# Optimization experiments

Measured on AMD Instinct MI355X. Metric: run time of the kernel, lower is better.

The kernel has to match this reference:

```python
import jax, jax.numpy as jnp
import numpy as np

N = 100000
E = 1600000
IN_CH = 128
HEADS = 4
OUT_CH = 32
NEG_SLOPE = 0.2


def setup_inputs() -> dict:
    key = jax.random.key(0)
    k1, k2, k3, k4 = jax.random.split(key, 4)
    x = jax.random.normal(k1, (N, IN_CH), dtype=jnp.float32)
    edge_index = jax.random.randint(k2, (2, E), 0, N, dtype=jnp.int64)
    # xavier-uniform-like init scales
    w_lim = float(np.sqrt(6.0 / (IN_CH + HEADS * OUT_CH)))
    a_lim = float(np.sqrt(6.0 / (HEADS + 2 * OUT_CH)))
    weight = jax.random.uniform(k3, (IN_CH, HEADS * OUT_CH), dtype=jnp.float32, minval=-w_lim, maxval=w_lim)
    att = jax.random.uniform(k4, (1, HEADS, 2 * OUT_CH), dtype=jnp.float32, minval=-a_lim, maxval=a_lim)
    bias = jnp.zeros((HEADS * OUT_CH,), dtype=jnp.float32)
    return {"x": x, "edge_index": edge_index, "weight": weight, "att": att, "bias": bias}


def reference(x, edge_index, weight, att, bias):
    n = x.shape[0]
    h = jnp.matmul(x, weight).reshape(n, HEADS, OUT_CH)  # [N, H, C]
    src, dst = edge_index[0], edge_index[1]
    x_src = h[src]  # [E, H, C]
    x_dst = h[dst]  # [E, H, C]
    # att is [1, H, 2C]; split so we never materialize the concat tensor
    att_src = att[:, :, :OUT_CH]  # [1, H, C]
    att_dst = att[:, :, OUT_CH:]  # [1, H, C]
    alpha = (x_src * att_src).sum(-1) + (x_dst * att_dst).sum(-1)  # [E, H]
    alpha = jnp.where(alpha >= 0, alpha, NEG_SLOPE * alpha)  # leaky_relu
    # segment softmax over edges grouped by dst
    seg_max = jax.ops.segment_max(alpha, dst, num_segments=n)  # [N, H]
    alpha = jnp.exp(alpha - seg_max[dst])
    seg_sum = jax.ops.segment_sum(alpha, dst, num_segments=n)  # [N, H]
    alpha = alpha / (seg_sum[dst] + 1e-16)
    # scatter-add weighted messages
    out = jax.ops.segment_sum(alpha[:, :, None] * x_src, dst, num_segments=n)  # [N, H, C]
    out = out.reshape(n, HEADS * OUT_CH)  # concat=True
    return out + bias
```

## Files before the change

### kernel.cpp

```cpp
#include <hip/hip_runtime.h>

#define N_NODES 100000
#define N_EDGES 1600000
#define IN_CH   128
#define HEADS   4
#define OUT_CH  32
#define HID     128
#define NEG_SLOPE 0.2f

#define BNODES  1024
#define NBUCK   ((N_NODES + BNODES - 1) / BNODES)
#define NBLK    256
#define EPB     (N_EDGES / NBLK)

typedef unsigned int  uint;
typedef unsigned short ushort;

__device__ __forceinline__ ushort f2bf(float f) {
    uint u = __float_as_uint(f);
    return (ushort)((u + 0x7FFFu + ((u >> 16) & 1u)) >> 16);
}

#define BM 64
#define BK 32
__global__ __launch_bounds__(256) void k_gemm(const float* __restrict__ x,
                                              const float* __restrict__ w,
                                              ushort* __restrict__ h) {
    __shared__ float xs[BK][BM + 4];
    __shared__ float wsld[BK][HID + 4];

    const int tid  = threadIdx.x;
    const int nodeBase = blockIdx.x * BM;
    const int c0 = (tid & 15) * 8;
    const int n0 = (tid >> 4) * 4;

    float acc[4][8];
#pragma unroll
    for (int i = 0; i < 4; i++)
#pragma unroll
        for (int j = 0; j < 8; j++) acc[i][j] = 0.0f;

    for (int k0 = 0; k0 < IN_CH; k0 += BK) {
#pragma unroll
        for (int l = 0; l < 2; l++) {
            int idx  = tid + l * 256;
            int row  = idx >> 3;
            int col4 = (idx & 7) * 4;
            int n = nodeBase + row;
            float4 v = make_float4(0.f, 0.f, 0.f, 0.f);
            if (n < N_NODES) v = *reinterpret_cast<const float4*>(x + (size_t)n * IN_CH + k0 + col4);
            xs[col4 + 0][row] = v.x;
            xs[col4 + 1][row] = v.y;
            xs[col4 + 2][row] = v.z;
            xs[col4 + 3][row] = v.w;
        }
#pragma unroll
        for (int l = 0; l < 4; l++) {
            int idx  = tid + l * 256;
            int row  = idx >> 5;
            int col4 = (idx & 31) * 4;
            float4 v = *reinterpret_cast<const float4*>(w + (size_t)(k0 + row) * HID + col4);
            *reinterpret_cast<float4*>(&wsld[row][col4]) = v;
        }
        __syncthreads();

#pragma unroll
        for (int kk = 0; kk < BK; kk++) {
            float4 xv = *reinterpret_cast<const float4*>(&xs[kk][n0]);
            float4 wa = *reinterpret_cast<const float4*>(&wsld[kk][c0]);
            float4 wb = *reinterpret_cast<const float4*>(&wsld[kk][c0 + 4]);
            float xr[4] = {xv.x, xv.y, xv.z, xv.w};
            float wr[8] = {wa.x, wa.y, wa.z, wa.w, wb.x, wb.y, wb.z, wb.w};
#pragma unroll
            for (int i = 0; i < 4; i++)
#pragma unroll
                for (int j = 0; j < 8; j++)
                    acc[i][j] = fmaf(xr[i], wr[j], acc[i][j]);
        }
        __syncthreads();
    }

#pragma unroll
    for (int i = 0; i < 4; i++) {
        int n = nodeBase + n0 + i;
        if (n < N_NODES) {
            uint4 pk;
            pk.x = (uint)f2bf(acc[i][0]) | ((uint)f2bf(acc[i][1]) << 16);
            pk.y = (uint)f2bf(acc[i][2]) | ((uint)f2bf(acc[i][3]) << 16);
            pk.z = (uint)f2bf(acc[i][4]) | ((uint)f2bf(acc[i][5]) << 16);
            pk.w = (uint)f2bf(acc[i][6]) | ((uint)f2bf(acc[i][7]) << 16);
            *reinterpret_cast<uint4*>(h + (size_t)n * HID + c0) = pk;
        }
    }
}

__global__ void k_scores(const ushort* __restrict__ h, const float* __restrict__ att,
                         float* __restrict__ s_src, float* __restrict__ s_dst) {
    int i = blockIdx.x * blockDim.x + threadIdx.x;
    if (i >= N_NODES * HEADS) return;
    int head = i & (HEADS - 1);
    const uint* hp = reinterpret_cast<const uint*>(h + (size_t)i * OUT_CH);
    const float* as = att + head * (2 * OUT_CH);
    const float* ad = as + OUT_CH;
    float ss = 0.f, sd = 0.f;
#pragma unroll
    for (int q = 0; q < 4; q++) {
        uint4 u = reinterpret_cast<const uint4*>(hp)[q];
        uint uv[4] = {u.x, u.y, u.z, u.w};
#pragma unroll
        for (int t = 0; t < 4; t++) {
            int c = q * 8 + t * 2;
            float f0 = __uint_as_float(uv[t] << 16);
            float f1 = __uint_as_float(uv[t] & 0xFFFF0000u);
            ss += f0 * as[c] + f1 * as[c + 1];
            sd += f0 * ad[c] + f1 * ad[c + 1];
        }
    }
    s_src[i] = ss;
    s_dst[i] = sd;
}

__global__ __launch_bounds__(256) void k_h0(const int* __restrict__ ei,
                                            int* __restrict__ hist) {
    __shared__ int cnt[NBUCK];
    int t = threadIdx.x;
    if (t < NBUCK) cnt[t] = 0;
    __syncthreads();
    int base = blockIdx.x * EPB;
    for (int e = base + t; e < base + EPB; e += 256)
        atomicAdd(&cnt[ei[N_EDGES + e] >> 10], 1);
    __syncthreads();
    if (t < NBUCK) hist[blockIdx.x * NBUCK + t] = cnt[t];
}

__global__ __launch_bounds__(128) void k_sc0(int* __restrict__ hist,
                                             int* __restrict__ bucket_base) {
    __shared__ int sm[128];
    int t = threadIdx.x;
    int total = 0;
    if (t < NBUCK) {
#pragma unroll 8
        for (int r = 0; r < NBLK; r++) total += hist[r * NBUCK + t];
    }
    sm[t] = total;
    __syncthreads();
    for (int off = 1; off < 128; off <<= 1) {
        int v = (t >= off) ? sm[t - off] : 0;
        __syncthreads();
        sm[t] += v;
        __syncthreads();
    }
    int excl = sm[t] - total;
    if (t < NBUCK) {
        bucket_base[t] = excl;
        int running = excl;
#pragma unroll 8
        for (int r = 0; r < NBLK; r++) {
            int tmp = hist[r * NBUCK + t];
            hist[r * NBUCK + t] = running;
            running += tmp;
        }
    }
    if (t == 0) bucket_base[NBUCK] = N_EDGES;
}

__global__ __launch_bounds__(256) void k_b1(const int* __restrict__ ei,
                                            const int* __restrict__ hist,
                                            int* __restrict__ packed) {
    __shared__ int cur[NBUCK];
    int t = threadIdx.x;
    if (t < NBUCK) cur[t] = hist[blockIdx.x * NBUCK + t];
    __syncthreads();
    int base = blockIdx.x * EPB;
    for (int e = base + t; e < base + EPB; e += 256) {
        int src = ei[e], dst = ei[N_EDGES + e];
        int pos = atomicAdd(&cur[dst >> 10], 1);
        packed[pos] = (src << 10) | (dst & (BNODES - 1));
    }
}

__global__ __launch_bounds__(256) void k_b2(const int* __restrict__ packed,
                                            const int* __restrict__ bucket_base,
                                            int* __restrict__ csr_src,
                                            int* __restrict__ row_start) {
    __shared__ int cnt[BNODES];
    __shared__ int cur[BNODES];
    __shared__ int sm[256];
    int b = blockIdx.x, t = threadIdx.x;
    int beg = bucket_base[b], end = bucket_base[b + 1];
#pragma unroll
    for (int j = 0; j < 4; j++) cnt[t * 4 + j] = 0;
    __syncthreads();
    for (int e = beg + t; e < end; e += 256)
        atomicAdd(&cnt[packed[e] & (BNODES - 1)], 1);
    __syncthreads();
    int c0 = cnt[t * 4], c1 = cnt[t * 4 + 1], c2 = cnt[t * 4 + 2], c3 = cnt[t * 4 + 3];
    int tot = c0 + c1 + c2 + c3;
    sm[t] = tot;
    __syncthreads();
    for (int off = 1; off < 256; off <<= 1) {
        int v = (t >= off) ? sm[t - off] : 0;
        __syncthreads();
        sm[t] += v;
        __syncthreads();
    }
    int p0 = beg + sm[t] - tot;
    int p1 = p0 + c0, p2 = p1 + c1, p3 = p2 + c2;
    cur[t * 4] = p0; cur[t * 4 + 1] = p1; cur[t * 4 + 2] = p2; cur[t * 4 + 3] = p3;
    int nodeb = b * BNODES + t * 4;
    int pv[4] = {p0, p1, p2, p3};
#pragma unroll
    for (int j = 0; j < 4; j++)
        if (nodeb + j <= N_NODES) row_start[nodeb + j] = pv[j];
    __syncthreads();
    for (int e = beg + t; e < end; e += 256) {
        int pk = packed[e];
        int pos = atomicAdd(&cur[pk & (BNODES - 1)], 1);
        csr_src[pos] = pk >> 10;
    }
}

__global__ __launch_bounds__(256) void k_agg(const int* __restrict__ row_start,
                                             const int* __restrict__ csr_src,
                                             const float* __restrict__ s_src,
                                             const float* __restrict__ s_dst,
                                             const ushort* __restrict__ h,
                                             const float* __restrict__ bias,
                                             float* __restrict__ out) {
    const int n    = blockIdx.x * 4 + (threadIdx.x >> 6);
    const int lane = threadIdx.x & 63;
    const int g    = lane >> 4;
    const int q    = lane & 15;
    const int head = q >> 2;

    const float sdh = s_dst[n * HEADS + head];
    const int beg = row_start[n], end = row_start[n + 1];
    const uint4* __restrict__ hrow = reinterpret_cast<const uint4*>(h);

    float acc[8];
#pragma unroll
    for (int k = 0; k < 8; k++) acc[k] = 0.f;
    float sum_w = 0.f;

#pragma unroll 2
    for (int j = beg; j < end; j += 4) {
        int e = j + g;
        bool valid = e < end;
        int src = csr_src[valid ? e : end - 1];
        float ss = s_src[src * HEADS + head];
        uint4 u = hrow[(size_t)src * (HID / 8) + q];
        float a = ss + sdh;
        a = fmaxf(a, NEG_SLOPE * a);
        float wgt = valid ? __expf(a) : 0.f;
        sum_w += wgt;
        uint uv[4] = {u.x, u.y, u.z, u.w};
#pragma unroll
        for (int t = 0; t < 4; t++) {
            acc[2 * t]     = fmaf(wgt, __uint_as_float(uv[t] << 16),        acc[2 * t]);
            acc[2 * t + 1] = fmaf(wgt, __uint_as_float(uv[t] & 0xFFFF0000u), acc[2 * t + 1]);
        }
    }

#pragma unroll
    for (int k = 0; k < 8; k++) {
        acc[k] += __shfl_xor(acc[k], 16);
        acc[k] += __shfl_xor(acc[k], 32);
    }
    sum_w += __shfl_xor(sum_w, 16);
    sum_w += __shfl_xor(sum_w, 32);

    if (g == 0) {
        float inv = 1.0f / (sum_w + 1e-16f);
        int ch = q * 8;
        float4 b0 = *reinterpret_cast<const float4*>(bias + ch);
        float4 b1 = *reinterpret_cast<const float4*>(bias + ch + 4);
        float4 o0, o1;
        o0.x = acc[0] * inv + b0.x; o0.y = acc[1] * inv + b0.y;
        o0.z = acc[2] * inv + b0.z; o0.w = acc[3] * inv + b0.w;
        o1.x = acc[4] * inv + b1.x; o1.y = acc[5] * inv + b1.y;
        o1.z = acc[6] * inv + b1.z; o1.w = acc[7] * inv + b1.w;
        *reinterpret_cast<float4*>(out + (size_t)n * HID + ch)     = o0;
        *reinterpret_cast<float4*>(out + (size_t)n * HID + ch + 4) = o1;
    }
}

extern "C" void kernel_launch(void* const* d_in, const int* in_sizes, int n_in,
                              void* d_out, int out_size, void* d_ws, size_t ws_size,
                              hipStream_t stream) {
    const float* x    = (const float*)d_in[0];
    const int*   ei   = (const int*)  d_in[1];
    const float* w    = (const float*)d_in[2];
    const float* att  = (const float*)d_in[3];
    const float* bias = (const float*)d_in[4];
    float* out = (float*)d_out;

    char* p = (char*)d_ws;
    float* s_src    = (float*)p;  p += (size_t)N_NODES * HEADS * 4;
    float* s_dst    = (float*)p;  p += (size_t)N_NODES * HEADS * 4;
    ushort* h       = (ushort*)p; p += (size_t)N_NODES * HID * 2;
    int* csr_src    = (int*)p;    p += (size_t)N_EDGES * 4;
    int* packed     = (int*)p;    p += (size_t)N_EDGES * 4;
    int* hist       = (int*)p;    p += (size_t)NBLK * NBUCK * 4;
    int* row_start  = (int*)p;    p += (size_t)(N_NODES + 1) * 4;
    int* bucket_base= (int*)p;    p += (size_t)(NBUCK + 1) * 4;

    k_gemm<<<(N_NODES + BM - 1) / BM, 256, 0, stream>>>(x, w, h);
    k_scores<<<(N_NODES * HEADS + 255) / 256, 256, 0, stream>>>(h, att, s_src, s_dst);
    k_h0<<<NBLK, 256, 0, stream>>>(ei, hist);
    k_sc0<<<1, 128, 0, stream>>>(hist, bucket_base);
    k_b1<<<NBLK, 256, 0, stream>>>(ei, hist, packed);
    k_b2<<<NBUCK, 256, 0, stream>>>(packed, bucket_base, csr_src, row_start);
    k_agg<<<N_NODES / 4, 256, 0, stream>>>(row_start, csr_src, s_src, s_dst, h, bias, out);
}
```

Measured before the change: 319.4 us.

## Fuse attention scores into GEMM and replace histogram-scan bucketing with padded atomic slots

Attention score dot products are now computed in the GEMM epilogue from fp32 accumulators, using a shuffle reduction, which removes the separate score kernel and its re-read of h. The three-kernel bucket sort (histogram, single-block scan, scatter) becomes one scatter kernel. Each block reserves space in fixed-size padded bucket slots through a global atomic, and k_b2 recomputes the tight offsets with a small scan. This cuts the launch count from seven to four and removes the serial single-block scan. The cost is that edge order inside a bucket becomes nondeterministic, and correctness depends on no bucket exceeding BSLOT edges. Scores are also now taken from fp32 values instead of the bf16-rounded h.

```diff
diff --git a/kernel.cpp b/kernel.cpp
--- a/kernel.cpp
+++ b/kernel.cpp
@@ -12,6 +12,7 @@
 #define NBUCK   ((N_NODES + BNODES - 1) / BNODES)
 #define NBLK    256
 #define EPB     (N_EDGES / NBLK)
+#define BSLOT   18432
 
 typedef unsigned int  uint;
 typedef unsigned short ushort;
@@ -25,7 +26,11 @@
 #define BK 32
 __global__ __launch_bounds__(256) void k_gemm(const float* __restrict__ x,
                                               const float* __restrict__ w,
-                                              ushort* __restrict__ h) {
+                                              const float* __restrict__ att,
+                                              ushort* __restrict__ h,
+                                              float* __restrict__ s_src,
+                                              float* __restrict__ s_dst,
+                                              int* __restrict__ bucket_cnt) {
     __shared__ float xs[BK][BM + 4];
     __shared__ float wsld[BK][HID + 4];
 
@@ -33,6 +38,8 @@
     const int nodeBase = blockIdx.x * BM;
     const int c0 = (tid & 15) * 8;
     const int n0 = (tid >> 4) * 4;
+
+    if (blockIdx.x == 0 && tid < NBUCK) bucket_cnt[tid] = 0;
 
     float acc[4][8];
 #pragma unroll
@@ -92,37 +99,39 @@
             *reinterpret_cast<uint4*>(h + (size_t)n * HID + c0) = pk;
         }
     }
-}
-
-__global__ void k_scores(const ushort* __restrict__ h, const float* __restrict__ att,
-                         float* __restrict__ s_src, float* __restrict__ s_dst) {
-    int i = blockIdx.x * blockDim.x + threadIdx.x;
-    if (i >= N_NODES * HEADS) return;
-    int head = i & (HEADS - 1);
-    const uint* hp = reinterpret_cast<const uint*>(h + (size_t)i * OUT_CH);
-    const float* as = att + head * (2 * OUT_CH);
-    const float* ad = as + OUT_CH;
-    float ss = 0.f, sd = 0.f;
-#pragma unroll
-    for (int q = 0; q < 4; q++) {
-        uint4 u = reinterpret_cast<const uint4*>(hp)[q];
-        uint uv[4] = {u.x, u.y, u.z, u.w};
-#pragma unroll
-        for (int t = 0; t < 4; t++) {
-            int c = q * 8 + t * 2;
-            float f0 = __uint_as_float(uv[t] << 16);
-            float f1 = __uint_as_float(uv[t] & 0xFFFF0000u);
-            ss += f0 * as[c] + f1 * as[c + 1];
-            sd += f0 * ad[c] + f1 * ad[c + 1];
-        }
-    }
-    s_src[i] = ss;
-    s_dst[i] = sd;
-}
-
-__global__ __launch_bounds__(256) void k_h0(const int* __restrict__ ei,
-                                            int* __restrict__ hist) {
+
+    {
+        const int head = c0 >> 5;
+        const int cb   = c0 & 31;
+        const float* as = att + head * (2 * OUT_CH) + cb;
+        const float* ad = as + OUT_CH;
+        float av[8], dv[8];
+#pragma unroll
+        for (int j = 0; j < 8; j++) { av[j] = as[j]; dv[j] = ad[j]; }
+#pragma unroll
+        for (int i = 0; i < 4; i++) {
+            float ps = 0.f, pd = 0.f;
+#pragma unroll
+            for (int j = 0; j < 8; j++) {
+                ps = fmaf(acc[i][j], av[j], ps);
+                pd = fmaf(acc[i][j], dv[j], pd);
+            }
+            ps += __shfl_xor(ps, 1);  ps += __shfl_xor(ps, 2);
+            pd += __shfl_xor(pd, 1);  pd += __shfl_xor(pd, 2);
+            int n = nodeBase + n0 + i;
+            if ((tid & 3) == 0 && n < N_NODES) {
+                s_src[n * HEADS + head] = ps;
+                s_dst[n * HEADS + head] = pd;
+            }
+        }
+    }
+}
+
+__global__ __launch_bounds__(256) void k_scatter(const int* __restrict__ ei,
+                                                 int* __restrict__ bucket_cnt,
+                                                 int* __restrict__ packed) {
     __shared__ int cnt[NBUCK];
+    __shared__ int cur[NBUCK];
     int t = threadIdx.x;
     if (t < NBUCK) cnt[t] = 0;
     __syncthreads();
@@ -130,48 +139,11 @@
     for (int e = base + t; e < base + EPB; e += 256)
         atomicAdd(&cnt[ei[N_EDGES + e] >> 10], 1);
     __syncthreads();
-    if (t < NBUCK) hist[blockIdx.x * NBUCK + t] = cnt[t];
-}
-
-__global__ __launch_bounds__(128) void k_sc0(int* __restrict__ hist,
-                                             int* __restrict__ bucket_base) {
-    __shared__ int sm[128];
-    int t = threadIdx.x;
-    int total = 0;
     if (t < NBUCK) {
-#pragma unroll 8
-        for (int r = 0; r < NBLK; r++) total += hist[r * NBUCK + t];
-    }
-    sm[t] = total;
-    __syncthreads();
-    for (int off = 1; off < 128; off <<= 1) {
-        int v = (t >= off) ? sm[t - off] : 0;
-        __syncthreads();
-        sm[t] += v;
-        __syncthreads();
-    }
-    int excl = sm[t] - total;
-    if (t < NBUCK) {
-        bucket_base[t] = excl;
-        int running = excl;
-#pragma unroll 8
-        for (int r = 0; r < NBLK; r++) {
-            int tmp = hist[r * NBUCK + t];
-            hist[r * NBUCK + t] = running;
-            running += tmp;
-        }
-    }
-    if (t == 0) bucket_base[NBUCK] = N_EDGES;
-}
-
-__global__ __launch_bounds__(256) void k_b1(const int* __restrict__ ei,
-                                            const int* __restrict__ hist,
-                                            int* __restrict__ packed) {
-    __shared__ int cur[NBUCK];
-    int t = threadIdx.x;
-    if (t < NBUCK) cur[t] = hist[blockIdx.x * NBUCK + t];
-    __syncthreads();
-    int base = blockIdx.x * EPB;
+        int myBase = atomicAdd(&bucket_cnt[t], cnt[t]);
+        cur[t] = t * BSLOT + myBase;
+    }
+    __syncthreads();
     for (int e = base + t; e < base + EPB; e += 256) {
         int src = ei[e], dst = ei[N_EDGES + e];
         int pos = atomicAdd(&cur[dst >> 10], 1);
@@ -180,18 +152,32 @@
 }
 
 __global__ __launch_bounds__(256) void k_b2(const int* __restrict__ packed,
-                                            const int* __restrict__ bucket_base,
+                                            const int* __restrict__ bucket_cnt,
                                             int* __restrict__ csr_src,
                                             int* __restrict__ row_start) {
     __shared__ int cnt[BNODES];
     __shared__ int cur[BNODES];
     __shared__ int sm[256];
     int b = blockIdx.x, t = threadIdx.x;
-    int beg = bucket_base[b], end = bucket_base[b + 1];
+
+    sm[t] = (t < NBUCK) ? bucket_cnt[t] : 0;
+    __syncthreads();
+    for (int off = 1; off < 256; off <<= 1) {
+        int v = (t >= off) ? sm[t - off] : 0;
+        __syncthreads();
+        sm[t] += v;
+        __syncthreads();
+    }
+    int myCnt     = bucket_cnt[b];
+    int tight_beg = sm[b] - myCnt;
+    int beg_pad   = b * BSLOT;
+    int end_pad   = beg_pad + myCnt;
+    __syncthreads();
+
 #pragma unroll
     for (int j = 0; j < 4; j++) cnt[t * 4 + j] = 0;
     __syncthreads();
-    for (int e = beg + t; e < end; e += 256)
+    for (int e = beg_pad + t; e < end_pad; e += 256)
         atomicAdd(&cnt[packed[e] & (BNODES - 1)], 1);
     __syncthreads();
     int c0 = cnt[t * 4], c1 = cnt[t * 4 + 1], c2 = cnt[t * 4 + 2], c3 = cnt[t * 4 + 3];
@@ -204,7 +190,7 @@
         sm[t] += v;
         __syncthreads();
     }
-    int p0 = beg + sm[t] - tot;
+    int p0 = tight_beg + sm[t] - tot;
     int p1 = p0 + c0, p2 = p1 + c1, p3 = p2 + c2;
     cur[t * 4] = p0; cur[t * 4 + 1] = p1; cur[t * 4 + 2] = p2; cur[t * 4 + 3] = p3;
     int nodeb = b * BNODES + t * 4;
@@ -213,7 +199,7 @@
     for (int j = 0; j < 4; j++)
         if (nodeb + j <= N_NODES) row_start[nodeb + j] = pv[j];
     __syncthreads();
-    for (int e = beg + t; e < end; e += 256) {
+    for (int e = beg_pad + t; e < end_pad; e += 256) {
         int pk = packed[e];
         int pos = atomicAdd(&cur[pk & (BNODES - 1)], 1);
         csr_src[pos] = pk >> 10;
@@ -299,16 +285,12 @@
     float* s_dst    = (float*)p;  p += (size_t)N_NODES * HEADS * 4;
     ushort* h       = (ushort*)p; p += (size_t)N_NODES * HID * 2;
     int* csr_src    = (int*)p;    p += (size_t)N_EDGES * 4;
-    int* packed     = (int*)p;    p += (size_t)N_EDGES * 4;
-    int* hist       = (int*)p;    p += (size_t)NBLK * NBUCK * 4;
+    int* packed     = (int*)p;    p += (size_t)NBUCK * BSLOT * 4;
     int* row_start  = (int*)p;    p += (size_t)(N_NODES + 1) * 4;
-    int* bucket_base= (int*)p;    p += (size_t)(NBUCK + 1) * 4;
-
-    k_gemm<<<(N_NODES + BM - 1) / BM, 256, 0, stream>>>(x, w, h);
-    k_scores<<<(N_NODES * HEADS + 255) / 256, 256, 0, stream>>>(h, att, s_src, s_dst);
-    k_h0<<<NBLK, 256, 0, stream>>>(ei, hist);
-    k_sc0<<<1, 128, 0, stream>>>(hist, bucket_base);
-    k_b1<<<NBLK, 256, 0, stream>>>(ei, hist, packed);
-    k_b2<<<NBUCK, 256, 0, stream>>>(packed, bucket_base, csr_src, row_start);
+    int* bucket_cnt = (int*)p;    p += (size_t)NBUCK * 4;
+
+    k_gemm<<<(N_NODES + BM - 1) / BM, 256, 0, stream>>>(x, w, att, h, s_src, s_dst, bucket_cnt);
+    k_scatter<<<NBLK, 256, 0, stream>>>(ei, bucket_cnt, packed);
+    k_b2<<<NBUCK, 256, 0, stream>>>(packed, bucket_cnt, csr_src, row_start);
     k_agg<<<N_NODES / 4, 256, 0, stream>>>(row_start, csr_src, s_src, s_dst, h, bias, out);
 }
```

New measurement: 301.8 us. 1.06x faster.
